# Kernel optimization log

Hardware: AMD Instinct MI355X
Metric: run time of the kernel (lower is better)

Reference implementation:

```python
import jax, jax.numpy as jnp
import numpy as np

B, N, M, D = 32, 1024, 576, 768

def setup_inputs() -> dict:
    key = jax.random.key(0)
    k1, k2 = jax.random.split(key)
    hidden_states = jax.random.normal(k1, (B, N, D), dtype=jnp.float32)
    img_hidden_state = jax.random.normal(k2, (B, M, D), dtype=jnp.float32)
    return {"hidden_states": hidden_states, "img_hidden_state": img_hidden_state}

def reference(hidden_states, img_hidden_state):
    # Unscaled cross-attention: softmax(Q K^T) V with Q=text, K=V=image features.
    scores = jnp.einsum('bnd,bmd->bnm', hidden_states, img_hidden_state)  # [B,N,M]
    probs = jax.nn.softmax(scores, axis=-1)
    fusion_output = jnp.einsum('bnm,bmd->bnd', probs, img_hidden_state)   # [B,N,D]
    return fusion_output
```

## Files before the change

### kernel.cpp

```cpp
#include <hip/hip_runtime.h>

typedef float f32x4 __attribute__((ext_vector_type(4)));
typedef _Float16 h8 __attribute__((ext_vector_type(8)));
typedef unsigned short us8 __attribute__((ext_vector_type(8)));

#define DEV __device__ __forceinline__
#define SBARRIER() asm volatile("s_barrier" ::: "memory")
#define LGKM0()    asm volatile("s_waitcnt lgkmcnt(0)" ::: "memory")
#define VMCNT3()   asm volatile("s_waitcnt vmcnt(3)" ::: "memory")
#define VMCNT0()   asm volatile("s_waitcnt vmcnt(0)" ::: "memory")
#define SCHED0()   __builtin_amdgcn_sched_barrier(0)

constexpr int Bb = 32, Nn = 1024, Mm = 576, Dd = 768;
constexpr float L2E = 1.44269504088896340736f;

constexpr size_t KF_ELEMS = (size_t)Bb * 36 * 24 * 512;

DEV unsigned short f2h(float x) {
  _Float16 h = (_Float16)x;
  return __builtin_bit_cast(unsigned short, h);
}
DEV void gll16(const void* g, void* l) {
  __builtin_amdgcn_global_load_lds(
      (const __attribute__((address_space(1))) void*)g,
      (__attribute__((address_space(3))) void*)l, 16, 0, 0);
}

__global__ __launch_bounds__(256)
void fusion_prep(const float* __restrict__ K, unsigned short* __restrict__ Kf,
                 unsigned short* __restrict__ Vf)
{
  const int t = threadIdx.x;
  const int b = blockIdx.x / 24, dc = blockIdx.x % 24;
  const int l = t & 63;
  {
    const int lt = t >> 6;
    const int ro = l & 15, go = l >> 4;
#pragma unroll
    for (int it = 0; it < 9; ++it) {
      const int kvt = it * 4 + lt;
      const float* src = K + ((size_t)(b * Mm + kvt * 16 + ro)) * Dd + dc * 32 + go * 8;
      f32x4 v0 = *(const f32x4*)src;
      f32x4 v1 = *(const f32x4*)(src + 4);
      us8 h;
      h[0]=f2h(v0[0]); h[1]=f2h(v0[1]); h[2]=f2h(v0[2]); h[3]=f2h(v0[3]);
      h[4]=f2h(v1[0]); h[5]=f2h(v1[1]); h[6]=f2h(v1[2]); h[7]=f2h(v1[3]);
      *(us8*)&Kf[(((size_t)((b * 36 + kvt) * 24 + dc)) << 9) + l * 8] = h;
    }
  }
  {
    const int kch = t >> 7;
    const int dtl = (t >> 6) & 1;
    const int d = dc * 32 + dtl * 16 + (l & 15);
    const int kvo = (l >> 4) * 8;
#pragma unroll
    for (int it = 0; it < 9; ++it) {
      const int kc = it * 2 + kch;
      const int kv0 = kc * 32 + kvo;
      us8 o;
#pragma unroll
      for (int j = 0; j < 8; ++j)
        o[j] = f2h(K[((size_t)(b * Mm + kv0 + j)) * Dd + d]);
      *(us8*)&Vf[(((size_t)((b * 18 + kc) * 48 + dc * 2 + dtl)) << 9) + l * 8] = o;
    }
  }
}

__global__ __launch_bounds__(1024, 1)
void fusion_main(const float* __restrict__ Q, const unsigned short* __restrict__ Kf,
                 const unsigned short* __restrict__ Vf, float* __restrict__ Out)
{
  __shared__ alignas(16) unsigned char lds[147456];
  __shared__ float sRa[4][128];
  __shared__ float sRb[4][128];

  const int tid  = threadIdx.x;
  const int lane = tid & 63;
  const int w    = tid >> 6;
  const int g    = lane >> 4;
  const int ln   = lane & 15;
  const int wq   = w >> 2;
  const int wkv  = w & 3;
  const int wq2  = w >> 3;
  const int wd8  = w & 7;

  const bool loader  = (w < 12);
  const bool qstager = (w >= 12);

  const int bid = blockIdx.x;
  const int xcd = bid & 7, ii = bid >> 3;
  const int b  = (xcd << 2) | (ii >> 3);
  const int q0 = (ii & 7) * 128;

  const float* Qb = Q + ((size_t)(b * Nn + q0)) * Dd;
  const unsigned char* KfB = (const unsigned char*)Kf + ((size_t)(b * 36 * 24) << 10);
  const unsigned short* VfB = Vf + ((size_t)(b * 18 * 48) << 9);

  const int u0 = w * 3;
  const int t256 = tid & 255;
  const int s0 = t256, s1 = t256 + 256;
  const int qt0 = s0 >> 6, l0 = s0 & 63;
  const int qt1 = s1 >> 6, l1 = s1 & 63;
  const float* qsrc0 = Qb + (size_t)(qt0 * 16 + (l0 & 15)) * Dd + (l0 >> 4) * 8;
  const float* qsrc1 = Qb + (size_t)(qt1 * 16 + (l1 & 15)) * Dd + (l1 >> 4) * 8;
  unsigned char* qd0 = lds + 110592 + qt0 * 1024 + l0 * 16;
  unsigned char* qd1 = lds + 110592 + qt1 * 1024 + l1 * 16;

  {
    f32x4 a0, a1, b0, b1;
    if (qstager) {
      a0 = *(const f32x4*)qsrc0; a1 = *(const f32x4*)(qsrc0 + 4);
      b0 = *(const f32x4*)qsrc1; b1 = *(const f32x4*)(qsrc1 + 4);
    }
    SCHED0();
    if (loader) {
#pragma unroll
      for (int j = 0; j < 3; ++j)
        gll16(KfB + ((size_t)((u0 + j) * 24) << 10) + (lane << 4), lds + (u0 + j) * 1024);
#pragma unroll
      for (int j = 0; j < 3; ++j)
        gll16(KfB + ((size_t)((u0 + j) * 24 + 1) << 10) + (lane << 4), lds + 36864 + (u0 + j) * 1024);
    }
    if (qstager) {
      us8 h0, h1;
#pragma unroll
      for (int k = 0; k < 4; ++k) {
        h0[k]   = f2h(a0[k] * L2E);
        h0[k+4] = f2h(a1[k] * L2E);
        h1[k]   = f2h(b0[k] * L2E);
        h1[k+4] = f2h(b1[k] * L2E);
      }
      *(us8*)qd0 = h0;
      *(us8*)qd1 = h1;
    }
    if (loader) { VMCNT3(); }
    LGKM0();
    SBARRIER();
    SCHED0();
  }

  f32x4 acc[2][9];
#pragma unroll
  for (int mt = 0; mt < 2; ++mt)
#pragma unroll
    for (int nt = 0; nt < 9; ++nt) acc[mt][nt] = (f32x4){0.f, 0.f, 0.f, 0.f};

#pragma unroll 1
  for (int c = 0; c < 24; ++c) {
    f32x4 a0, a1, b0, b1;
    if (qstager && c < 23) {
      const size_t off = (size_t)(c + 1) * 32;
      a0 = *(const f32x4*)(qsrc0 + off); a1 = *(const f32x4*)(qsrc0 + off + 4);
      b0 = *(const f32x4*)(qsrc1 + off); b1 = *(const f32x4*)(qsrc1 + off + 4);
    }
    SCHED0();
    if (loader && c < 22) {
      unsigned char* dst = lds + ((c + 2) % 3) * 36864;
#pragma unroll
      for (int j = 0; j < 3; ++j) {
        const int u = u0 + j;
        gll16(KfB + ((size_t)(u * 24 + c + 2) << 10) + (lane << 4), dst + u * 1024);
      }
    }
    const unsigned char* qb = lds + 110592 + (c & 1) * 8192;
    const unsigned char* kb = lds + (c % 3) * 36864;
    h8 qh[2];
#pragma unroll
    for (int mt = 0; mt < 2; ++mt)
      qh[mt] = *(const h8*)(qb + (wq * 2 + mt) * 1024 + lane * 16);
    __builtin_amdgcn_s_setprio(1);
#pragma unroll
    for (int nt = 0; nt < 9; ++nt) {
      const h8 kf = *(const h8*)(kb + (wkv * 9 + nt) * 1024 + lane * 16);
#pragma unroll
      for (int mt = 0; mt < 2; ++mt)
        acc[mt][nt] = __builtin_amdgcn_mfma_f32_16x16x32_f16(qh[mt], kf, acc[mt][nt], 0, 0, 0);
    }
    __builtin_amdgcn_s_setprio(0);
    SCHED0();
    if (qstager && c < 23) {
      us8 h0, h1;
#pragma unroll
      for (int k = 0; k < 4; ++k) {
        h0[k]   = f2h(a0[k] * L2E);
        h0[k+4] = f2h(a1[k] * L2E);
        h1[k]   = f2h(b0[k] * L2E);
        h1[k+4] = f2h(b1[k] * L2E);
      }
      *(us8*)(qd0 + ((c + 1) & 1) * 8192) = h0;
      *(us8*)(qd1 + ((c + 1) & 1) * 8192) = h1;
    }
    if (loader) {
      if (c <= 21) { VMCNT3(); }
      else         { VMCNT0(); }
    }
    LGKM0();
    SBARRIER();
    SCHED0();
  }

  float pm[2][4];
#pragma unroll
  for (int mt = 0; mt < 2; ++mt)
#pragma unroll
    for (int i2 = 0; i2 < 4; ++i2) {
      float v = acc[mt][0][i2];
#pragma unroll
      for (int nt = 1; nt < 9; ++nt) v = fmaxf(v, acc[mt][nt][i2]);
      pm[mt][i2] = v;
    }
#pragma unroll
  for (int mk = 1; mk < 16; mk <<= 1)
#pragma unroll
    for (int mt = 0; mt < 2; ++mt)
#pragma unroll
      for (int i2 = 0; i2 < 4; ++i2)
        pm[mt][i2] = fmaxf(pm[mt][i2], __shfl_xor(pm[mt][i2], mk, 64));
  if (ln == 0) {
#pragma unroll
    for (int mt = 0; mt < 2; ++mt)
#pragma unroll
      for (int i2 = 0; i2 < 4; ++i2)
        sRa[wkv][wq * 32 + mt * 16 + g * 4 + i2] = pm[mt][i2];
  }
  __syncthreads();

  float mfin[2][4], ps[2][4];
#pragma unroll
  for (int mt = 0; mt < 2; ++mt)
#pragma unroll
    for (int i2 = 0; i2 < 4; ++i2) {
      const int rw = wq * 32 + mt * 16 + g * 4 + i2;
      mfin[mt][i2] = fmaxf(fmaxf(sRa[0][rw], sRa[1][rw]), fmaxf(sRa[2][rw], sRa[3][rw]));
      ps[mt][i2] = 0.f;
    }
#pragma unroll
  for (int mt = 0; mt < 2; ++mt)
#pragma unroll
    for (int nt = 0; nt < 9; ++nt)
#pragma unroll
      for (int i2 = 0; i2 < 4; ++i2) {
        const float p = exp2f(acc[mt][nt][i2] - mfin[mt][i2]);
        acc[mt][nt][i2] = p;
        ps[mt][i2] += p;
      }
#pragma unroll
  for (int mk = 1; mk < 16; mk <<= 1)
#pragma unroll
    for (int mt = 0; mt < 2; ++mt)
#pragma unroll
      for (int i2 = 0; i2 < 4; ++i2)
        ps[mt][i2] += __shfl_xor(ps[mt][i2], mk, 64);
  if (ln == 0) {
#pragma unroll
    for (int mt = 0; mt < 2; ++mt)
#pragma unroll
      for (int i2 = 0; i2 < 4; ++i2)
        sRb[wkv][wq * 32 + mt * 16 + g * 4 + i2] = ps[mt][i2];
  }
  __syncthreads();

  {
    unsigned short* sPp = (unsigned short*)lds;
#pragma unroll
    for (int mt = 0; mt < 2; ++mt)
#pragma unroll
      for (int i2 = 0; i2 < 4; ++i2) {
        const int rw = wq * 32 + mt * 16 + g * 4 + i2;
        const float inv = 1.0f / ((sRb[0][rw] + sRb[1][rw]) + (sRb[2][rw] + sRb[3][rw]));
#pragma unroll
        for (int nt = 0; nt < 9; ++nt) {
          const int u = wkv * 18 + nt * 2 + (ln >> 3);
          sPp[rw * 576 + ((u ^ (rw & 7)) << 3) + (ln & 7)] = f2h(acc[mt][nt][i2] * inv);
        }
      }
  }
  __syncthreads();

#pragma unroll 1
  for (int p = 0; p < 2; ++p) {
    f32x4 O[4][3];
#pragma unroll
    for (int mt = 0; mt < 4; ++mt)
#pragma unroll
      for (int nt = 0; nt < 3; ++nt) O[mt][nt] = (f32x4){0.f, 0.f, 0.f, 0.f};

    const unsigned short* vbase = VfB + ((size_t)(wd8 * 6 + p * 3) << 9) + lane * 8;
    h8 vfA[3], vfB2[3];
#pragma unroll
    for (int nt = 0; nt < 3; ++nt)
      vfA[nt] = *(const h8*)(vbase + ((size_t)nt << 9));

#pragma unroll 1
    for (int kc = 0; kc < 18; kc += 2) {
#pragma unroll
      for (int nt = 0; nt < 3; ++nt)
        vfB2[nt] = *(const h8*)(vbase + ((size_t)((kc + 1) * 48 + nt) << 9));
      {
        h8 pa[4];
#pragma unroll
        for (int mt = 0; mt < 4; ++mt) {
          const int row = wq2 * 64 + mt * 16 + ln;
          const int u = kc * 4 + g;
          pa[mt] = *(const h8*)(lds + row * 1152 + ((u ^ (row & 7)) << 4));
        }
#pragma unroll
        for (int nt = 0; nt < 3; ++nt)
#pragma unroll
          for (int mt = 0; mt < 4; ++mt)
            O[mt][nt] = __builtin_amdgcn_mfma_f32_16x16x32_f16(pa[mt], vfA[nt], O[mt][nt], 0, 0, 0);
      }
      if (kc < 16) {
#pragma unroll
        for (int nt = 0; nt < 3; ++nt)
          vfA[nt] = *(const h8*)(vbase + ((size_t)((kc + 2) * 48 + nt) << 9));
      }
      {
        h8 pa[4];
#pragma unroll
        for (int mt = 0; mt < 4; ++mt) {
          const int row = wq2 * 64 + mt * 16 + ln;
          const int u = (kc + 1) * 4 + g;
          pa[mt] = *(const h8*)(lds + row * 1152 + ((u ^ (row & 7)) << 4));
        }
#pragma unroll
        for (int nt = 0; nt < 3; ++nt)
#pragma unroll
          for (int mt = 0; mt < 4; ++mt)
            O[mt][nt] = __builtin_amdgcn_mfma_f32_16x16x32_f16(pa[mt], vfB2[nt], O[mt][nt], 0, 0, 0);
      }
    }

    float* ob = Out + ((size_t)(b * Nn + q0 + wq2 * 64)) * Dd;
#pragma unroll
    for (int mt = 0; mt < 4; ++mt)
#pragma unroll
      for (int nt = 0; nt < 3; ++nt)
#pragma unroll
        for (int i2 = 0; i2 < 4; ++i2)
          ob[(size_t)(mt * 16 + g * 4 + i2) * Dd + wd8 * 96 + p * 48 + nt * 16 + ln] = O[mt][nt][i2];
  }
}

extern "C" void kernel_launch(void* const* d_in, const int* in_sizes, int n_in,
                              void* d_out, int out_size, void* d_ws, size_t ws_size,
                              hipStream_t stream) {
  const float* Q = (const float*)d_in[0];
  const float* K = (const float*)d_in[1];
  float* Out = (float*)d_out;
  unsigned short* Kf = (unsigned short*)d_ws;
  unsigned short* Vf = Kf + KF_ELEMS;
  fusion_prep<<<dim3(Bb * 24), dim3(256), 0, stream>>>(K, Kf, Vf);
  fusion_main<<<dim3(Bb * 8), dim3(1024), 0, stream>>>(Q, Kf, Vf, Out);
}
```

Before: 119.7 us.

## Load Q directly into registers and double-buffer K in two-chunk stages

Removes the separate Q-staging waves that converted Q to fp16 in LDS. Each wave now loads its own Q fragments from global memory into registers and converts them on the fly. K loading is spread across all 16 waves and moves to a double-buffered scheme that processes two 32-wide d-chunks per barrier, so the loop runs 12 iterations instead of 24 and needs half as many barriers. The cost is more register pressure from the Q prefetch registers, redundant Q global loads across the waves that share a Q row, and plain __syncthreads in place of hand-tuned waitcnt/barrier control, which may serialize loads behind compute.

```diff
diff --git a/kernel.cpp b/kernel.cpp
--- a/kernel.cpp
+++ b/kernel.cpp
@@ -5,11 +5,6 @@
 typedef unsigned short us8 __attribute__((ext_vector_type(8)));
 
 #define DEV __device__ __forceinline__
-#define SBARRIER() asm volatile("s_barrier" ::: "memory")
-#define LGKM0()    asm volatile("s_waitcnt lgkmcnt(0)" ::: "memory")
-#define VMCNT3()   asm volatile("s_waitcnt vmcnt(3)" ::: "memory")
-#define VMCNT0()   asm volatile("s_waitcnt vmcnt(0)" ::: "memory")
-#define SCHED0()   __builtin_amdgcn_sched_barrier(0)
 
 constexpr int Bb = 32, Nn = 1024, Mm = 576, Dd = 768;
 constexpr float L2E = 1.44269504088896340736f;
@@ -84,9 +79,6 @@
   const int wq2  = w >> 3;
   const int wd8  = w & 7;
 
-  const bool loader  = (w < 12);
-  const bool qstager = (w >= 12);
-
   const int bid = blockIdx.x;
   const int xcd = bid & 7, ii = bid >> 3;
   const int b  = (xcd << 2) | (ii >> 3);
@@ -96,48 +88,30 @@
   const unsigned char* KfB = (const unsigned char*)Kf + ((size_t)(b * 36 * 24) << 10);
   const unsigned short* VfB = Vf + ((size_t)(b * 18 * 48) << 9);
 
-  const int u0 = w * 3;
-  const int t256 = tid & 255;
-  const int s0 = t256, s1 = t256 + 256;
-  const int qt0 = s0 >> 6, l0 = s0 & 63;
-  const int qt1 = s1 >> 6, l1 = s1 & 63;
-  const float* qsrc0 = Qb + (size_t)(qt0 * 16 + (l0 & 15)) * Dd + (l0 >> 4) * 8;
-  const float* qsrc1 = Qb + (size_t)(qt1 * 16 + (l1 & 15)) * Dd + (l1 >> 4) * 8;
-  unsigned char* qd0 = lds + 110592 + qt0 * 1024 + l0 * 16;
-  unsigned char* qd1 = lds + 110592 + qt1 * 1024 + l1 * 16;
-
-  {
-    f32x4 a0, a1, b0, b1;
-    if (qstager) {
-      a0 = *(const f32x4*)qsrc0; a1 = *(const f32x4*)(qsrc0 + 4);
-      b0 = *(const f32x4*)qsrc1; b1 = *(const f32x4*)(qsrc1 + 4);
-    }
-    SCHED0();
-    if (loader) {
-#pragma unroll
-      for (int j = 0; j < 3; ++j)
-        gll16(KfB + ((size_t)((u0 + j) * 24) << 10) + (lane << 4), lds + (u0 + j) * 1024);
-#pragma unroll
-      for (int j = 0; j < 3; ++j)
-        gll16(KfB + ((size_t)((u0 + j) * 24 + 1) << 10) + (lane << 4), lds + 36864 + (u0 + j) * 1024);
-    }
-    if (qstager) {
-      us8 h0, h1;
-#pragma unroll
-      for (int k = 0; k < 4; ++k) {
-        h0[k]   = f2h(a0[k] * L2E);
-        h0[k+4] = f2h(a1[k] * L2E);
-        h1[k]   = f2h(b0[k] * L2E);
-        h1[k+4] = f2h(b1[k] * L2E);
-      }
-      *(us8*)qd0 = h0;
-      *(us8*)qd1 = h1;
-    }
-    if (loader) { VMCNT3(); }
-    LGKM0();
-    SBARRIER();
-    SCHED0();
-  }
+  const int nu = (w < 8) ? 5 : 4;
+  const int u0 = (w < 8) ? w * 5 : 40 + (w - 8) * 4;
+
+  const float* qp[2];
+  qp[0] = Qb + (size_t)(wq * 32 + ln) * Dd + g * 8;
+  qp[1] = qp[0] + (size_t)16 * Dd;
+
+  f32x4 qvA[2][2][2], qvB[2][2][2];
+#pragma unroll
+  for (int mt = 0; mt < 2; ++mt)
+#pragma unroll
+    for (int cc = 0; cc < 2; ++cc) {
+      qvA[mt][cc][0] = *(const f32x4*)(qp[mt] + cc * 32);
+      qvA[mt][cc][1] = *(const f32x4*)(qp[mt] + cc * 32 + 4);
+    }
+#pragma unroll
+  for (int j = 0; j < 5; ++j)
+    if (j < nu) {
+      const int u = u0 + j;
+      const int cc = u / 36, uu = u % 36;
+      gll16(KfB + ((size_t)(uu * 24 + cc) << 10) + (lane << 4),
+            lds + cc * 36864 + uu * 1024);
+    }
+  __syncthreads();
 
   f32x4 acc[2][9];
 #pragma unroll
@@ -146,57 +120,59 @@
     for (int nt = 0; nt < 9; ++nt) acc[mt][nt] = (f32x4){0.f, 0.f, 0.f, 0.f};
 
 #pragma unroll 1
-  for (int c = 0; c < 24; ++c) {
-    f32x4 a0, a1, b0, b1;
-    if (qstager && c < 23) {
-      const size_t off = (size_t)(c + 1) * 32;
-      a0 = *(const f32x4*)(qsrc0 + off); a1 = *(const f32x4*)(qsrc0 + off + 4);
-      b0 = *(const f32x4*)(qsrc1 + off); b1 = *(const f32x4*)(qsrc1 + off + 4);
-    }
-    SCHED0();
-    if (loader && c < 22) {
-      unsigned char* dst = lds + ((c + 2) % 3) * 36864;
-#pragma unroll
-      for (int j = 0; j < 3; ++j) {
-        const int u = u0 + j;
-        gll16(KfB + ((size_t)(u * 24 + c + 2) << 10) + (lane << 4), dst + u * 1024);
-      }
-    }
-    const unsigned char* qb = lds + 110592 + (c & 1) * 8192;
-    const unsigned char* kb = lds + (c % 3) * 36864;
-    h8 qh[2];
-#pragma unroll
-    for (int mt = 0; mt < 2; ++mt)
-      qh[mt] = *(const h8*)(qb + (wq * 2 + mt) * 1024 + lane * 16);
-    __builtin_amdgcn_s_setprio(1);
-#pragma unroll
-    for (int nt = 0; nt < 9; ++nt) {
-      const h8 kf = *(const h8*)(kb + (wkv * 9 + nt) * 1024 + lane * 16);
+  for (int i = 0; i < 12; ++i) {
+    const bool stg = (i < 11);
+    if (stg) {
 #pragma unroll
       for (int mt = 0; mt < 2; ++mt)
-        acc[mt][nt] = __builtin_amdgcn_mfma_f32_16x16x32_f16(qh[mt], kf, acc[mt][nt], 0, 0, 0);
-    }
-    __builtin_amdgcn_s_setprio(0);
-    SCHED0();
-    if (qstager && c < 23) {
-      us8 h0, h1;
-#pragma unroll
-      for (int k = 0; k < 4; ++k) {
-        h0[k]   = f2h(a0[k] * L2E);
-        h0[k+4] = f2h(a1[k] * L2E);
-        h1[k]   = f2h(b0[k] * L2E);
-        h1[k+4] = f2h(b1[k] * L2E);
-      }
-      *(us8*)(qd0 + ((c + 1) & 1) * 8192) = h0;
-      *(us8*)(qd1 + ((c + 1) & 1) * 8192) = h1;
-    }
-    if (loader) {
-      if (c <= 21) { VMCNT3(); }
-      else         { VMCNT0(); }
-    }
-    LGKM0();
-    SBARRIER();
-    SCHED0();
+#pragma unroll
+        for (int cc = 0; cc < 2; ++cc) {
+          const size_t off = (size_t)(i + 1) * 64 + cc * 32;
+          qvB[mt][cc][0] = *(const f32x4*)(qp[mt] + off);
+          qvB[mt][cc][1] = *(const f32x4*)(qp[mt] + off + 4);
+        }
+      unsigned char* dstb = lds + ((i + 1) & 1) * 73728;
+#pragma unroll
+      for (int j = 0; j < 5; ++j)
+        if (j < nu) {
+          const int u = u0 + j;
+          const int cc = u / 36, uu = u % 36;
+          gll16(KfB + ((size_t)(uu * 24 + 2 * i + 2 + cc) << 10) + (lane << 4),
+                dstb + cc * 36864 + uu * 1024);
+        }
+    }
+    const unsigned char* kbb = lds + (i & 1) * 73728;
+#pragma unroll
+    for (int cc = 0; cc < 2; ++cc) {
+      h8 qh[2];
+#pragma unroll
+      for (int mt = 0; mt < 2; ++mt)
+#pragma unroll
+        for (int k = 0; k < 4; ++k) {
+          qh[mt][k]     = (_Float16)(qvA[mt][cc][0][k] * L2E);
+          qh[mt][k + 4] = (_Float16)(qvA[mt][cc][1][k] * L2E);
+        }
+      const unsigned char* kb = kbb + cc * 36864;
+      __builtin_amdgcn_s_setprio(1);
+#pragma unroll
+      for (int nt = 0; nt < 9; ++nt) {
+        const h8 kf = *(const h8*)(kb + (wkv * 9 + nt) * 1024 + lane * 16);
+#pragma unroll
+        for (int mt = 0; mt < 2; ++mt)
+          acc[mt][nt] = __builtin_amdgcn_mfma_f32_16x16x32_f16(qh[mt], kf, acc[mt][nt], 0, 0, 0);
+      }
+      __builtin_amdgcn_s_setprio(0);
+    }
+    if (stg) {
+#pragma unroll
+      for (int mt = 0; mt < 2; ++mt)
+#pragma unroll
+        for (int cc = 0; cc < 2; ++cc) {
+          qvA[mt][cc][0] = qvB[mt][cc][0];
+          qvA[mt][cc][1] = qvB[mt][cc][1];
+        }
+    }
+    __syncthreads();
   }
 
   float pm[2][4];
```

Result: slower. 302.9 us (+153.2%).
